# Kernel optimization log

Measured on AMD Instinct MI355X. Metric: run time of the kernel, lower is better.

Reference implementation:

```python
import jax, jax.numpy as jnp
import numpy as np

MAX_ABS = 1.0          # assumed get_max_abs('T')
DT = 0.01              # forward default dt
TWO_PI = 2.0 * np.pi
B, D, N = 4096, 2048, 4096


def setup_inputs() -> dict:
    key = jax.random.key(0)
    k0, k1 = jax.random.split(key, 2)
    x = jax.random.normal(k0, (B, D), dtype=jnp.float32)
    # nn.Linear params
    W = jax.random.normal(k1, (N, D), dtype=jnp.float32) * (1.0 / np.sqrt(D))
    b = jnp.zeros((N,), dtype=jnp.float32)
    # oscillator params (as initialized in __init__)
    amplitude = jnp.ones((N,), dtype=jnp.float32)
    frequency = jnp.ones((N,), dtype=jnp.float32)
    phase_offset = jnp.zeros((N,), dtype=jnp.float32)
    damping = jnp.full((N,), 0.01, dtype=jnp.float32)
    return {"x": x, "W": W, "b": b, "amplitude": amplitude,
            "frequency": frequency, "phase_offset": phase_offset,
            "damping": damping}


def reference(x, W, b, amplitude, frequency, phase_offset, damping):
    # driving force: [B, N]
    force = x @ W.T + b
    omega_sq = (TWO_PI * frequency) ** 2  # [N]
    # t starts at 0 and is incremented ONCE per forward call
    t = DT

    def step(carry, f):
        state, vel = carry
        accel = -omega_sq * state - damping * vel + f
        vel = vel + accel * DT
        state = state + vel * DT
        return (state, vel), state

    init = (jnp.zeros((N,), x.dtype), jnp.zeros((N,), x.dtype))
    (_, _), states = jax.lax.scan(step, init, force)  # states: [B, N]

    # sinusoid term is identical for every batch step (t fixed within forward)
    osc = amplitude * jnp.sin(TWO_PI * frequency * t + phase_offset)  # [N]
    out = jnp.clip(states + osc, -MAX_ABS, MAX_ABS)
    return out
```

## Files before the change

### kernel.cpp

```cpp
#include <hip/hip_runtime.h>
#include <hip/hip_bf16.h>
#include <math.h>

#define MDIM 4096
#define KDIM 2048
#define NDIM 4096
#define DT   0.01f
#define TWO_PI_F 6.283185307179586f
#define CH 64
#define CL 64

typedef __attribute__((ext_vector_type(8))) short bf16x8;
typedef __attribute__((ext_vector_type(4))) float f32x4;

__device__ __forceinline__ unsigned short f2bf(float f) {
  unsigned int u = __float_as_uint(f);
  u += 0x7FFFu + ((u >> 16) & 1u);
  return (unsigned short)(u >> 16);
}
__device__ __forceinline__ float bf2f(unsigned short u) {
  return __uint_as_float(((unsigned int)u) << 16);
}

__global__ void cast2_bf16_kernel(const float* __restrict__ s0,
                                  unsigned short* __restrict__ d0,
                                  const float* __restrict__ s1,
                                  unsigned short* __restrict__ d1,
                                  int n4each) {
  int i = blockIdx.x * blockDim.x + threadIdx.x;
  const float4* sp;
  ushort4* dp;
  int j;
  if (i < n4each) { sp = (const float4*)s0; dp = (ushort4*)d0; j = i; }
  else            { sp = (const float4*)s1; dp = (ushort4*)d1; j = i - n4each; }
  float4 v = sp[j];
  ushort4 o;
  o.x = f2bf(v.x); o.y = f2bf(v.y); o.z = f2bf(v.z); o.w = f2bf(v.w);
  dp[j] = o;
}

__global__ __launch_bounds__(256, 2) void gemm_scan_kernel(
    const unsigned short* __restrict__ A,
    const unsigned short* __restrict__ Bm,
    const float* __restrict__ bias,
    const float* __restrict__ freq,
    const float* __restrict__ damp,
    unsigned short* __restrict__ zpart,
    float* __restrict__ chunkS,
    float* __restrict__ chunkV) {
  __shared__ __align__(16) unsigned short smem[16384];
  unsigned short* sA = smem;
  unsigned short* sB = smem + 4096;

  const int tid  = threadIdx.x;
  const int lane = tid & 63;
  const int wave = tid >> 6;
  const int wr = wave >> 1;
  const int wc = wave & 1;
  const int q  = lane >> 4;
  const int lm = lane & 15;

  const int bM = blockIdx.x * 128;
  const int bN = blockIdx.y * 128;

  f32x4 acc[4][4];
#pragma unroll
  for (int i = 0; i < 4; i++)
#pragma unroll
    for (int j = 0; j < 4; j++) acc[i][j] = (f32x4){0.f, 0.f, 0.f, 0.f};

  const int idx0 = tid;
  const int idx1 = tid + 256;
  const int r0 = idx0 >> 2, g0 = idx0 & 3;
  const int r1 = idx1 >> 2, g1 = idx1 & 3;
  const int dst0 = r0 * 32 + ((g0 ^ ((r0 >> 1) & 3)) * 8);
  const int dst1 = r1 * 32 + ((g1 ^ ((r1 >> 1) & 3)) * 8);
  const unsigned short* gA0 = A  + (size_t)(bM + r0) * KDIM + g0 * 8;
  const unsigned short* gA1 = A  + (size_t)(bM + r1) * KDIM + g1 * 8;
  const unsigned short* gB0 = Bm + (size_t)(bN + r0) * KDIM + g0 * 8;
  const unsigned short* gB1 = Bm + (size_t)(bN + r1) * KDIM + g1 * 8;
  const int rq = (q ^ ((lm >> 1) & 3)) * 8;

  for (int k0 = 0; k0 < KDIM; k0 += 32) {
    uint4 av0 = *(const uint4*)(gA0 + k0);
    uint4 av1 = *(const uint4*)(gA1 + k0);
    uint4 bv0 = *(const uint4*)(gB0 + k0);
    uint4 bv1 = *(const uint4*)(gB1 + k0);
    __syncthreads();
    *(uint4*)&sA[dst0] = av0;
    *(uint4*)&sA[dst1] = av1;
    *(uint4*)&sB[dst0] = bv0;
    *(uint4*)&sB[dst1] = bv1;
    __syncthreads();

    bf16x8 af[4], bfr[4];
#pragma unroll
    for (int mt = 0; mt < 4; mt++)
      af[mt]  = *(const bf16x8*)&sA[(wr * 64 + mt * 16 + lm) * 32 + rq];
#pragma unroll
    for (int nt = 0; nt < 4; nt++)
      bfr[nt] = *(const bf16x8*)&sB[(wc * 64 + nt * 16 + lm) * 32 + rq];

#pragma unroll
    for (int mt = 0; mt < 4; mt++)
#pragma unroll
      for (int nt = 0; nt < 4; nt++)
        acc[mt][nt] = __builtin_amdgcn_mfma_f32_16x16x32_bf16(
            af[mt], bfr[nt], acc[mt][nt], 0, 0, 0);
  }

  __syncthreads();
  unsigned short* sT = smem + wave * 4096;
#pragma unroll
  for (int nt = 0; nt < 4; nt++) {
    const float bz = bias[bN + wc * 64 + nt * 16 + lm];
#pragma unroll
    for (int mt = 0; mt < 4; mt++)
#pragma unroll
      for (int r = 0; r < 4; r++)
        sT[(mt * 16 + q * 4 + r) * 64 + nt * 16 + lm] =
            f2bf(acc[mt][nt][r] + bz);
  }
  __syncthreads();

  const int gcol = bN + wc * 64 + lane;
  const float om  = TWO_PI_F * freq[gcol];
  const float osq = om * om;
  const float dp  = damp[gcol];
  float s = 0.f, v = 0.f;
#pragma unroll 8
  for (int i = 0; i < CL; i++) {
    float f = bf2f(sT[i * 64 + lane]);
    v += (-osq * s - dp * v + f) * DT;
    s += v * DT;
    sT[i * 64 + lane] = f2bf(s);
  }
  const int chunk = 2 * blockIdx.x + wr;
  chunkS[chunk * NDIM + gcol] = s;
  chunkV[chunk * NDIM + gcol] = v;
  __syncthreads();

#pragma unroll
  for (int k = 0; k < 8; k++) {
    int slot = lane + 64 * k;
    int row  = slot >> 3;
    int col8 = (slot & 7) * 8;
    *(uint4*)&zpart[(size_t)(bM + wr * 64 + row) * NDIM + bN + wc * 64 + col8] =
        *(uint4*)&sT[row * 64 + col8];
  }
}

__global__ void scan_out_kernel(const unsigned short* __restrict__ zpart,
                                const float* __restrict__ amp,
                                const float* __restrict__ freq,
                                const float* __restrict__ phase,
                                const float* __restrict__ damp,
                                const float* __restrict__ chunkS,
                                const float* __restrict__ chunkV,
                                float* __restrict__ out) {
  int gid = blockIdx.x * blockDim.x + threadIdx.x;
  int n4 = gid & (NDIM / 4 - 1);
  int c  = gid >> 10;
  int n  = n4 * 4;

  float4 fr = *(const float4*)&freq[n];
  float4 dv = *(const float4*)&damp[n];
  float4 am = *(const float4*)&amp[n];
  float4 ph = *(const float4*)&phase[n];
  float omv[4] = {TWO_PI_F * fr.x, TWO_PI_F * fr.y, TWO_PI_F * fr.z, TWO_PI_F * fr.w};
  float dpv[4] = {dv.x, dv.y, dv.z, dv.w};
  float amv[4] = {am.x, am.y, am.z, am.w};
  float phv[4] = {ph.x, ph.y, ph.z, ph.w};
  float m00[4], m01[4], m10[4], m11[4];
  float p00[4], p01[4], p10[4], p11[4];
  float osc[4];
#pragma unroll
  for (int j = 0; j < 4; j++) {
    float osq = omv[j] * omv[j];
    m00[j] = 1.f - osq * DT * DT;  m01[j] = DT * (1.f - dpv[j] * DT);
    m10[j] = -osq * DT;            m11[j] = 1.f - dpv[j] * DT;
    p00[j] = m00[j]; p01[j] = m01[j]; p10[j] = m10[j]; p11[j] = m11[j];
    osc[j] = amv[j] * sinf(omv[j] * DT + phv[j]);
  }
#pragma unroll
  for (int i = 0; i < 6; i++)
#pragma unroll
    for (int j = 0; j < 4; j++) {
      float b00 = p00[j] * p00[j] + p01[j] * p10[j];
      float b01 = p00[j] * p01[j] + p01[j] * p11[j];
      float b10 = p10[j] * p00[j] + p11[j] * p10[j];
      float b11 = p10[j] * p01[j] + p11[j] * p11[j];
      p00[j] = b00; p01[j] = b01; p10[j] = b10; p11[j] = b11;
    }

  float hs[4] = {0.f, 0.f, 0.f, 0.f}, hv[4] = {0.f, 0.f, 0.f, 0.f};
  for (int cc = 0; cc < c; cc++) {
    float4 ls = *(const float4*)&chunkS[cc * NDIM + n];
    float4 lv = *(const float4*)&chunkV[cc * NDIM + n];
    float lsv[4] = {ls.x, ls.y, ls.z, ls.w};
    float lvv[4] = {lv.x, lv.y, lv.z, lv.w};
#pragma unroll
    for (int j = 0; j < 4; j++) {
      float t = p00[j] * hs[j] + p01[j] * hv[j] + lsv[j];
      float u = p10[j] * hs[j] + p11[j] * hv[j] + lvv[j];
      hs[j] = t; hv[j] = u;
    }
  }

  const unsigned short* zp = zpart + (size_t)c * CL * NDIM + n;
  float* op = out + (size_t)c * CL * NDIM + n;
#pragma unroll 4
  for (int i = 0; i < CL; i++) {
    ushort4 zv = *(const ushort4*)&zp[(size_t)i * NDIM];
    float z[4] = {bf2f(zv.x), bf2f(zv.y), bf2f(zv.z), bf2f(zv.w)};
    float o[4];
#pragma unroll
    for (int j = 0; j < 4; j++) {
      float t = m00[j] * hs[j] + m01[j] * hv[j];
      float u = m10[j] * hs[j] + m11[j] * hv[j];
      hs[j] = t; hv[j] = u;
      o[j] = fminf(1.f, fmaxf(-1.f, hs[j] + z[j] + osc[j]));
    }
    *(float4*)&op[(size_t)i * NDIM] = (float4){o[0], o[1], o[2], o[3]};
  }
}

__global__ __launch_bounds__(256, 2) void gemm_bt_kernel(
    const unsigned short* __restrict__ A,
    const unsigned short* __restrict__ Bm,
    const float* __restrict__ bias,
    unsigned short* __restrict__ C) {
  __shared__ __align__(16) unsigned short sA[128 * 32];
  __shared__ __align__(16) unsigned short sB[128 * 32];

  const int tid  = threadIdx.x;
  const int lane = tid & 63;
  const int wave = tid >> 6;
  const int wr = wave >> 1;
  const int wc = wave & 1;
  const int q  = lane >> 4;
  const int lm = lane & 15;

  const int bM = blockIdx.x * 128;
  const int bN = blockIdx.y * 128;

  f32x4 acc[4][4];
#pragma unroll
  for (int i = 0; i < 4; i++)
#pragma unroll
    for (int j = 0; j < 4; j++) acc[i][j] = (f32x4){0.f, 0.f, 0.f, 0.f};

  const int idx0 = tid;
  const int idx1 = tid + 256;
  const int r0 = idx0 >> 2, g0 = idx0 & 3;
  const int r1 = idx1 >> 2, g1 = idx1 & 3;
  const int dst0 = r0 * 32 + ((g0 ^ ((r0 >> 1) & 3)) * 8);
  const int dst1 = r1 * 32 + ((g1 ^ ((r1 >> 1) & 3)) * 8);
  const unsigned short* gA0 = A  + (size_t)(bM + r0) * KDIM + g0 * 8;
  const unsigned short* gA1 = A  + (size_t)(bM + r1) * KDIM + g1 * 8;
  const unsigned short* gB0 = Bm + (size_t)(bN + r0) * KDIM + g0 * 8;
  const unsigned short* gB1 = Bm + (size_t)(bN + r1) * KDIM + g1 * 8;
  const int rq = (q ^ ((lm >> 1) & 3)) * 8;

  for (int k0 = 0; k0 < KDIM; k0 += 32) {
    uint4 av0 = *(const uint4*)(gA0 + k0);
    uint4 av1 = *(const uint4*)(gA1 + k0);
    uint4 bv0 = *(const uint4*)(gB0 + k0);
    uint4 bv1 = *(const uint4*)(gB1 + k0);
    __syncthreads();
    *(uint4*)&sA[dst0] = av0;
    *(uint4*)&sA[dst1] = av1;
    *(uint4*)&sB[dst0] = bv0;
    *(uint4*)&sB[dst1] = bv1;
    __syncthreads();

    bf16x8 af[4], bfr[4];
#pragma unroll
    for (int mt = 0; mt < 4; mt++)
      af[mt]  = *(const bf16x8*)&sA[(wr * 64 + mt * 16 + lm) * 32 + rq];
#pragma unroll
    for (int nt = 0; nt < 4; nt++)
      bfr[nt] = *(const bf16x8*)&sB[(wc * 64 + nt * 16 + lm) * 32 + rq];

#pragma unroll
    for (int mt = 0; mt < 4; mt++)
#pragma unroll
      for (int nt = 0; nt < 4; nt++)
        acc[mt][nt] = __builtin_amdgcn_mfma_f32_16x16x32_bf16(
            af[mt], bfr[nt], acc[mt][nt], 0, 0, 0);
  }

#pragma unroll
  for (int nt = 0; nt < 4; nt++) {
    const int col = bN + wc * 64 + nt * 16 + lm;
    const float bz = bias[col];
#pragma unroll
    for (int mt = 0; mt < 4; mt++) {
      const int row0 = bM + wr * 64 + mt * 16 + q * 4;
#pragma unroll
      for (int r = 0; r < 4; r++)
        C[(size_t)(row0 + r) * NDIM + col] = f2bf(acc[mt][nt][r] + bz);
    }
  }
}

__global__ void scan_pass1(const unsigned short* __restrict__ force,
                           const float* __restrict__ freq,
                           const float* __restrict__ damp,
                           float* __restrict__ chunkS,
                           float* __restrict__ chunkV) {
  int gid = blockIdx.x * blockDim.x + threadIdx.x;
  int n4 = gid & (NDIM / 4 - 1);
  int c  = gid >> 10;
  int n  = n4 * 4;
  float4 fr = *(const float4*)&freq[n];
  float4 dv = *(const float4*)&damp[n];
  float osq[4] = {TWO_PI_F * fr.x, TWO_PI_F * fr.y, TWO_PI_F * fr.z, TWO_PI_F * fr.w};
  float dp[4]  = {dv.x, dv.y, dv.z, dv.w};
  float s[4] = {0.f, 0.f, 0.f, 0.f}, v[4] = {0.f, 0.f, 0.f, 0.f};
#pragma unroll
  for (int j = 0; j < 4; j++) osq[j] *= osq[j];
  const unsigned short* fp = force + (size_t)c * CL * NDIM + n;
#pragma unroll 4
  for (int i = 0; i < CL; i++) {
    ushort4 fv = *(const ushort4*)&fp[(size_t)i * NDIM];
    float f[4] = {bf2f(fv.x), bf2f(fv.y), bf2f(fv.z), bf2f(fv.w)};
#pragma unroll
    for (int j = 0; j < 4; j++) {
      float a = -osq[j] * s[j] - dp[j] * v[j] + f[j];
      v[j] += a * DT;
      s[j] += v[j] * DT;
    }
  }
  *(float4*)&chunkS[c * NDIM + n] = (float4){s[0], s[1], s[2], s[3]};
  *(float4*)&chunkV[c * NDIM + n] = (float4){v[0], v[1], v[2], v[3]};
}

__global__ void scan_pass2(const float* __restrict__ chunkS,
                           const float* __restrict__ chunkV,
                           const float* __restrict__ freq,
                           const float* __restrict__ damp,
                           float* __restrict__ carryS,
                           float* __restrict__ carryV) {
  int n = blockIdx.x * blockDim.x + threadIdx.x;
  float om = TWO_PI_F * freq[n];
  float osq = om * om;
  float dp = damp[n];
  float a00 = 1.f - osq * DT * DT, a01 = DT * (1.f - dp * DT);
  float a10 = -osq * DT,           a11 = 1.f - dp * DT;
#pragma unroll
  for (int i = 0; i < 6; i++) {
    float b00 = a00 * a00 + a01 * a10;
    float b01 = a00 * a01 + a01 * a11;
    float b10 = a10 * a00 + a11 * a10;
    float b11 = a10 * a01 + a11 * a11;
    a00 = b00; a01 = b01; a10 = b10; a11 = b11;
  }
  float cs = 0.f, cv = 0.f;
#pragma unroll 8
  for (int c = 0; c < CH; c++) {
    carryS[c * NDIM + n] = cs;
    carryV[c * NDIM + n] = cv;
    float ls = chunkS[c * NDIM + n];
    float lv = chunkV[c * NDIM + n];
    float ns = a00 * cs + a01 * cv + ls;
    float nv = a10 * cs + a11 * cv + lv;
    cs = ns; cv = nv;
  }
}

__global__ void scan_pass3(const unsigned short* __restrict__ force,
                           const float* __restrict__ amp,
                           const float* __restrict__ freq,
                           const float* __restrict__ phase,
                           const float* __restrict__ damp,
                           const float* __restrict__ carryS,
                           const float* __restrict__ carryV,
                           float* __restrict__ out) {
  int gid = blockIdx.x * blockDim.x + threadIdx.x;
  int n4 = gid & (NDIM / 4 - 1);
  int c  = gid >> 10;
  int n  = n4 * 4;
  float4 fr = *(const float4*)&freq[n];
  float4 dv = *(const float4*)&damp[n];
  float4 am = *(const float4*)&amp[n];
  float4 ph = *(const float4*)&phase[n];
  float om[4] = {TWO_PI_F * fr.x, TWO_PI_F * fr.y, TWO_PI_F * fr.z, TWO_PI_F * fr.w};
  float dp[4] = {dv.x, dv.y, dv.z, dv.w};
  float osq[4], osc[4], s[4], v[4];
  float amv[4] = {am.x, am.y, am.z, am.w};
  float phv[4] = {ph.x, ph.y, ph.z, ph.w};
#pragma unroll
  for (int j = 0; j < 4; j++) {
    osq[j] = om[j] * om[j];
    osc[j] = amv[j] * sinf(om[j] * DT + phv[j]);
  }
  float4 csv = *(const float4*)&carryS[c * NDIM + n];
  float4 cvv = *(const float4*)&carryV[c * NDIM + n];
  s[0] = csv.x; s[1] = csv.y; s[2] = csv.z; s[3] = csv.w;
  v[0] = cvv.x; v[1] = cvv.y; v[2] = cvv.z; v[3] = cvv.w;
  const unsigned short* fp = force + (size_t)c * CL * NDIM + n;
  float* op = out + (size_t)c * CL * NDIM + n;
#pragma unroll 4
  for (int i = 0; i < CL; i++) {
    ushort4 fv = *(const ushort4*)&fp[(size_t)i * NDIM];
    float f[4] = {bf2f(fv.x), bf2f(fv.y), bf2f(fv.z), bf2f(fv.w)};
    float o[4];
#pragma unroll
    for (int j = 0; j < 4; j++) {
      float a = -osq[j] * s[j] - dp[j] * v[j] + f[j];
      v[j] += a * DT;
      s[j] += v[j] * DT;
      o[j] = fminf(1.f, fmaxf(-1.f, s[j] + osc[j]));
    }
    *(float4*)&op[(size_t)i * NDIM] = (float4){o[0], o[1], o[2], o[3]};
  }
}

extern "C" void kernel_launch(void* const* d_in, const int* in_sizes, int n_in,
                              void* d_out, int out_size, void* d_ws, size_t ws_size,
                              hipStream_t stream) {
  const float* x     = (const float*)d_in[0];
  const float* W     = (const float*)d_in[1];
  const float* bias  = (const float*)d_in[2];
  const float* amp   = (const float*)d_in[3];
  const float* freq  = (const float*)d_in[4];
  const float* phase = (const float*)d_in[5];
  const float* damp  = (const float*)d_in[6];

  const size_t MiB = 1024 * 1024;
  const int n4each = MDIM * KDIM / 4;
  dim3 gg(MDIM / 128, NDIM / 128);

  if (ws_size >= 66 * MiB) {
    unsigned short* xbf   = (unsigned short*)d_ws;
    unsigned short* wbf   = xbf + (size_t)MDIM * KDIM;
    unsigned short* zpart = wbf + (size_t)NDIM * KDIM;
    float* chunkS = (float*)((char*)d_ws + 64 * MiB);
    float* chunkV = chunkS + CH * NDIM;

    cast2_bf16_kernel<<<(2 * n4each + 255) / 256, 256, 0, stream>>>(
        x, xbf, W, wbf, n4each);
    gemm_scan_kernel<<<gg, 256, 0, stream>>>(xbf, wbf, bias, freq, damp,
                                             zpart, chunkS, chunkV);
    scan_out_kernel<<<CH * NDIM / 4 / 256, 256, 0, stream>>>(
        zpart, amp, freq, phase, damp, chunkS, chunkV, (float*)d_out);
  } else {
    unsigned short* xbf   = (unsigned short*)d_ws;
    unsigned short* wbf   = xbf + (size_t)MDIM * KDIM;
    unsigned short* force = wbf + (size_t)NDIM * KDIM;
    float* chunkS = (float*)d_ws;
    float* chunkV = chunkS + CH * NDIM;
    float* carryS = chunkV + CH * NDIM;
    float* carryV = carryS + CH * NDIM;

    cast2_bf16_kernel<<<(2 * n4each + 255) / 256, 256, 0, stream>>>(
        x, xbf, W, wbf, n4each);
    gemm_bt_kernel<<<gg, 256, 0, stream>>>(xbf, wbf, bias, force);
    scan_pass1<<<CH * NDIM / 4 / 256, 256, 0, stream>>>(force, freq, damp,
                                                        chunkS, chunkV);
    scan_pass2<<<NDIM / 256, 256, 0, stream>>>(chunkS, chunkV, freq, damp,
                                               carryS, carryV);
    scan_pass3<<<CH * NDIM / 4 / 256, 256, 0, stream>>>(
        force, amp, freq, phase, damp, carryS, carryV, (float*)d_out);
  }
}
```

Measured before the change: 236.4 us.

## Compute chunk carries in a separate sequential pass instead of per-thread prefix

Adds a small kernel that runs a sequential scan over the chunk end-states for each column and writes the exclusive carry back into the chunk buffers in place. The output kernel then loads its carry directly rather than having each thread recompute the matrix power and rescan all preceding chunks, which is quadratic redundant work across chunks. The cost is an extra kernel launch and a serial 64-step pass over only 16 blocks.

```diff
diff --git a/kernel.cpp b/kernel.cpp
--- a/kernel.cpp
+++ b/kernel.cpp
@@ -150,14 +150,45 @@
   }
 }
 
-__global__ void scan_out_kernel(const unsigned short* __restrict__ zpart,
-                                const float* __restrict__ amp,
-                                const float* __restrict__ freq,
-                                const float* __restrict__ phase,
-                                const float* __restrict__ damp,
-                                const float* __restrict__ chunkS,
-                                const float* __restrict__ chunkV,
-                                float* __restrict__ out) {
+__global__ void scan_pass2_inplace(float* __restrict__ chunkS,
+                                   float* __restrict__ chunkV,
+                                   const float* __restrict__ freq,
+                                   const float* __restrict__ damp) {
+  int n = blockIdx.x * blockDim.x + threadIdx.x;
+  float om = TWO_PI_F * freq[n];
+  float osq = om * om;
+  float dp = damp[n];
+  float a00 = 1.f - osq * DT * DT, a01 = DT * (1.f - dp * DT);
+  float a10 = -osq * DT,           a11 = 1.f - dp * DT;
+#pragma unroll
+  for (int i = 0; i < 6; i++) {
+    float b00 = a00 * a00 + a01 * a10;
+    float b01 = a00 * a01 + a01 * a11;
+    float b10 = a10 * a00 + a11 * a10;
+    float b11 = a10 * a01 + a11 * a11;
+    a00 = b00; a01 = b01; a10 = b10; a11 = b11;
+  }
+  float cs = 0.f, cv = 0.f;
+#pragma unroll 8
+  for (int c = 0; c < CH; c++) {
+    float ls = chunkS[c * NDIM + n];
+    float lv = chunkV[c * NDIM + n];
+    chunkS[c * NDIM + n] = cs;
+    chunkV[c * NDIM + n] = cv;
+    float ns = a00 * cs + a01 * cv + ls;
+    float nv = a10 * cs + a11 * cv + lv;
+    cs = ns; cv = nv;
+  }
+}
+
+__global__ void scan_out_carry(const unsigned short* __restrict__ zpart,
+                               const float* __restrict__ amp,
+                               const float* __restrict__ freq,
+                               const float* __restrict__ phase,
+                               const float* __restrict__ damp,
+                               const float* __restrict__ carryS,
+                               const float* __restrict__ carryV,
+                               float* __restrict__ out) {
   int gid = blockIdx.x * blockDim.x + threadIdx.x;
   int n4 = gid & (NDIM / 4 - 1);
   int c  = gid >> 10;
@@ -171,41 +202,19 @@
   float dpv[4] = {dv.x, dv.y, dv.z, dv.w};
   float amv[4] = {am.x, am.y, am.z, am.w};
   float phv[4] = {ph.x, ph.y, ph.z, ph.w};
-  float m00[4], m01[4], m10[4], m11[4];
-  float p00[4], p01[4], p10[4], p11[4];
-  float osc[4];
+  float m00[4], m01[4], m10[4], m11[4], osc[4];
 #pragma unroll
   for (int j = 0; j < 4; j++) {
     float osq = omv[j] * omv[j];
     m00[j] = 1.f - osq * DT * DT;  m01[j] = DT * (1.f - dpv[j] * DT);
     m10[j] = -osq * DT;            m11[j] = 1.f - dpv[j] * DT;
-    p00[j] = m00[j]; p01[j] = m01[j]; p10[j] = m10[j]; p11[j] = m11[j];
     osc[j] = amv[j] * sinf(omv[j] * DT + phv[j]);
   }
-#pragma unroll
-  for (int i = 0; i < 6; i++)
-#pragma unroll
-    for (int j = 0; j < 4; j++) {
-      float b00 = p00[j] * p00[j] + p01[j] * p10[j];
-      float b01 = p00[j] * p01[j] + p01[j] * p11[j];
-      float b10 = p10[j] * p00[j] + p11[j] * p10[j];
-      float b11 = p10[j] * p01[j] + p11[j] * p11[j];
-      p00[j] = b00; p01[j] = b01; p10[j] = b10; p11[j] = b11;
-    }
-
-  float hs[4] = {0.f, 0.f, 0.f, 0.f}, hv[4] = {0.f, 0.f, 0.f, 0.f};
-  for (int cc = 0; cc < c; cc++) {
-    float4 ls = *(const float4*)&chunkS[cc * NDIM + n];
-    float4 lv = *(const float4*)&chunkV[cc * NDIM + n];
-    float lsv[4] = {ls.x, ls.y, ls.z, ls.w};
-    float lvv[4] = {lv.x, lv.y, lv.z, lv.w};
-#pragma unroll
-    for (int j = 0; j < 4; j++) {
-      float t = p00[j] * hs[j] + p01[j] * hv[j] + lsv[j];
-      float u = p10[j] * hs[j] + p11[j] * hv[j] + lvv[j];
-      hs[j] = t; hv[j] = u;
-    }
-  }
+
+  float4 csv = *(const float4*)&carryS[c * NDIM + n];
+  float4 cvv = *(const float4*)&carryV[c * NDIM + n];
+  float hs[4] = {csv.x, csv.y, csv.z, csv.w};
+  float hv[4] = {cvv.x, cvv.y, cvv.z, cvv.w};
 
   const unsigned short* zp = zpart + (size_t)c * CL * NDIM + n;
   float* op = out + (size_t)c * CL * NDIM + n;
@@ -443,7 +452,9 @@
         x, xbf, W, wbf, n4each);
     gemm_scan_kernel<<<gg, 256, 0, stream>>>(xbf, wbf, bias, freq, damp,
                                              zpart, chunkS, chunkV);
-    scan_out_kernel<<<CH * NDIM / 4 / 256, 256, 0, stream>>>(
+    scan_pass2_inplace<<<NDIM / 256, 256, 0, stream>>>(chunkS, chunkV,
+                                                       freq, damp);
+    scan_out_carry<<<CH * NDIM / 4 / 256, 256, 0, stream>>>(
         zpart, amp, freq, phase, damp, chunkS, chunkV, (float*)d_out);
   } else {
     unsigned short* xbf   = (unsigned short*)d_ws;
```

Result: faster. 224.0 us (-5.2%).
